# Kernel optimization log

Hardware: AMD Instinct MI355X
Metric: run time of the kernel (lower is better)

The kernel has to match this reference:

```python
import jax, jax.numpy as jnp
import numpy as np


def feature_map(x):
    # phi(x) = elu(x) + 1 (ensures positivity)
    return jax.nn.elu(x) + 1.0


def setup_inputs() -> dict:
    key = jax.random.key(0)
    k0, k1, k2, k3 = jax.random.split(key, 4)
    B, T, d_model, D = 4, 4096, 1024, 128
    x = jax.random.normal(k0, (B, T, d_model), dtype=jnp.float32)
    s = 1.0 / np.sqrt(d_model)
    Wq = jax.random.normal(k1, (d_model, D), dtype=jnp.float32) * s
    Wk = jax.random.normal(k2, (d_model, D), dtype=jnp.float32) * s
    Wv = jax.random.normal(k3, (d_model, D), dtype=jnp.float32) * s
    return {"x": x, "Wq": Wq, "Wk": Wk, "Wv": Wv}


def _causal_linear_attention(phi_q, phi_k, v):
    # phi_q, phi_k: [B,T,D]; v: [B,T,Dv]
    B, T, D = phi_q.shape
    Dv = v.shape[-1]
    # time-major for scan: [T,B,D]
    qT = jnp.swapaxes(phi_q, 0, 1)
    kT = jnp.swapaxes(phi_k, 0, 1)
    vT = jnp.swapaxes(v, 0, 1)

    def step(carry, inp):
        kv, ks = carry                       # kv: [B,D,Dv], ks: [B,D]
        qt, kt, vt = inp                     # each [B,D] / [B,Dv]
        kv = kv + kt[:, :, None] * vt[:, None, :]   # k_t^T v_t outer product
        ks = ks + kt
        num = jnp.einsum('bd,bdv->bv', qt, kv)      # [B,Dv]
        den = jnp.einsum('bd,bd->b', qt, ks)[:, None]
        return (kv, ks), num / den

    init = (jnp.zeros((B, D, Dv), phi_q.dtype), jnp.zeros((B, D), phi_q.dtype))
    _, outT = jax.lax.scan(step, init, (qT, kT, vT))  # outT: [T,B,Dv]
    return jnp.swapaxes(outT, 0, 1)


def reference(x, Wq, Wk, Wv):
    q = x @ Wq
    k = x @ Wk
    v = x @ Wv
    phi_q = feature_map(q)
    phi_k = feature_map(k)
    # dropout is identity in eval mode
    return _causal_linear_attention(phi_q, phi_k, v)
```

## Files before the change

### kernel.cpp

```cpp
#include <hip/hip_runtime.h>

#define DMODEL 1024
#define DHEAD 128
#define CHUNK 128
#define NCHUNK 32

typedef __attribute__((ext_vector_type(4))) float f32x4;
typedef __attribute__((ext_vector_type(8))) short bf16x8;

__device__ __forceinline__ unsigned short f2bf(float f) {
  union { float f; unsigned u; } v; v.f = f;
  unsigned r = v.u + 0x7FFF + ((v.u >> 16) & 1);
  return (unsigned short)(r >> 16);
}
__device__ __forceinline__ float bf2f(unsigned short h) {
  union { unsigned u; float f; } v; v.u = ((unsigned)h) << 16;
  return v.f;
}
__device__ __forceinline__ unsigned cvtpk(float lo, float hi) {
  unsigned r;
  asm("v_cvt_pk_bf16_f32 %0, %1, %2" : "=v"(r) : "v"(lo), "v"(hi));
  return r;
}
__device__ __forceinline__ void gload16(const void* g, void* l) {
  __builtin_amdgcn_global_load_lds(
      (const __attribute__((address_space(1))) unsigned int*)g,
      (__attribute__((address_space(3))) unsigned int*)l, 16, 0, 0);
}

__global__ __launch_bounds__(256) void transpose_w_kernel(
    const float* __restrict__ Wq, const float* __restrict__ Wk,
    const float* __restrict__ Wv, unsigned short* __restrict__ WT) {
  int id = blockIdx.x * 256 + threadIdx.x;
  int w = id >> 17;
  int rem = id & 131071;
  int n = rem >> 10;
  int k = rem & 1023;
  const float* W = (w == 0) ? Wq : (w == 1) ? Wk : Wv;
  WT[id] = f2bf(W[(size_t)k * DHEAD + n]);
}

__global__ __launch_bounds__(256) void proj_kernel(
    const float* __restrict__ x, const unsigned short* __restrict__ WT,
    unsigned short* __restrict__ phiQ, unsigned short* __restrict__ phiK,
    unsigned short* __restrict__ Vb) {
  const int which = blockIdx.y;
  const unsigned short* Wt = WT + (size_t)which * (DHEAD * DMODEL);
  unsigned short* outp = (which == 0) ? phiQ : (which == 1) ? phiK : Vb;
  const int m0 = blockIdx.x * 128;

  __shared__ float xs[128][32];
  __shared__ unsigned short ws[128][32];

  const int tid = threadIdx.x;
  const int wave = tid >> 6;
  const int lane = tid & 63;
  const int lrow = lane & 15, kgrp = lane >> 4;
  const int wr = wave >> 1, wc = wave & 1;

  f32x4 acc[4][4];
#pragma unroll
  for (int i = 0; i < 4; ++i)
#pragma unroll
    for (int j = 0; j < 4; ++j) acc[i][j] = (f32x4)0.0f;

  for (int kk = 0; kk < DMODEL; kk += 32) {
    if (kk) __syncthreads();
#pragma unroll
    for (int i = 0; i < 4; ++i) {
      int instr = i * 4 + wave;
      int row = instr * 8 + (lane >> 3);
      int slot = lane & 7;
      int gcol = (slot ^ (row & 7)) << 2;
      gload16(&x[(size_t)(m0 + row) * DMODEL + kk + gcol],
              (char*)xs + instr * 1024);
    }
#pragma unroll
    for (int i = 0; i < 2; ++i) {
      int instr = i * 4 + wave;
      int row = instr * 16 + (lane >> 2);
      int slot = lane & 3;
      int gcol = (slot ^ (row & 3)) << 3;
      gload16(&Wt[(size_t)row * DMODEL + kk + gcol],
              (char*)ws + instr * 1024);
    }
    __syncthreads();

    bf16x8 af[4];
#pragma unroll
    for (int mi = 0; mi < 4; ++mi) {
      int arow = wr * 64 + mi * 16 + lrow;
      int s0 = kgrp * 2;
      const float4 f0 = *reinterpret_cast<const float4*>(
          &xs[arow][(s0 ^ (arow & 7)) << 2]);
      const float4 f1 = *reinterpret_cast<const float4*>(
          &xs[arow][((s0 + 1) ^ (arow & 7)) << 2]);
      union { unsigned u[4]; bf16x8 v; } p;
      p.u[0] = cvtpk(f0.x, f0.y);
      p.u[1] = cvtpk(f0.z, f0.w);
      p.u[2] = cvtpk(f1.x, f1.y);
      p.u[3] = cvtpk(f1.z, f1.w);
      af[mi] = p.v;
    }
#pragma unroll
    for (int ni = 0; ni < 4; ++ni) {
      int brow = wc * 64 + ni * 16 + lrow;
      bf16x8 bf = *reinterpret_cast<const bf16x8*>(
          &ws[brow][(kgrp ^ (brow & 3)) << 3]);
#pragma unroll
      for (int mi = 0; mi < 4; ++mi)
        acc[mi][ni] = __builtin_amdgcn_mfma_f32_16x16x32_bf16(af[mi], bf, acc[mi][ni], 0, 0, 0);
    }
  }
#pragma unroll
  for (int mi = 0; mi < 4; ++mi)
#pragma unroll
    for (int ni = 0; ni < 4; ++ni)
#pragma unroll
      for (int r = 0; r < 4; ++r) {
        int row = m0 + wr * 64 + mi * 16 + kgrp * 4 + r;
        int col = wc * 64 + ni * 16 + lrow;
        float v = acc[mi][ni][r];
        if (which < 2) v = (v > 0.0f) ? (v + 1.0f) : __expf(v);
        outp[(size_t)row * DHEAD + col] = f2bf(v);
      }
}

__global__ __launch_bounds__(256) void chunkkv_kernel(
    const unsigned short* __restrict__ phiK, const unsigned short* __restrict__ Vb,
    float* __restrict__ KVc, float* __restrict__ ksc) {
  const size_t base = (size_t)blockIdx.x * CHUNK * DHEAD;
  __shared__ unsigned short kt[128][136];
  __shared__ unsigned short vt[128][136];
  __shared__ float csum[2][128];
  const int tid = threadIdx.x;
  const int wave = tid >> 6, lane = tid & 63;
  const int lrow = lane & 15, kgrp = lane >> 4;

  {
    int t = tid & 127, dp = tid >> 7;
#pragma unroll
    for (int i = 0; i < 8; ++i) {
      int d0 = (dp + 2 * i) * 8;
      uint4 k4 = *reinterpret_cast<const uint4*>(&phiK[base + (size_t)t * DHEAD + d0]);
      uint4 v4 = *reinterpret_cast<const uint4*>(&Vb[base + (size_t)t * DHEAD + d0]);
      const unsigned short* kp = reinterpret_cast<const unsigned short*>(&k4);
      const unsigned short* vp = reinterpret_cast<const unsigned short*>(&v4);
#pragma unroll
      for (int j = 0; j < 8; ++j) { kt[d0 + j][t] = kp[j]; vt[d0 + j][t] = vp[j]; }
    }
  }
  __syncthreads();

  f32x4 acc[2][8];
#pragma unroll
  for (int i = 0; i < 2; ++i)
#pragma unroll
    for (int j = 0; j < 8; ++j) acc[i][j] = (f32x4)0.0f;
#pragma unroll
  for (int ks = 0; ks < 4; ++ks) {
    int t0 = ks * 32 + kgrp * 8;
    bf16x8 afrag[2];
#pragma unroll
    for (int tr = 0; tr < 2; ++tr)
      afrag[tr] = *reinterpret_cast<const bf16x8*>(&vt[wave * 32 + tr * 16 + lrow][t0]);
#pragma unroll
    for (int tc = 0; tc < 8; ++tc) {
      bf16x8 bfrag = *reinterpret_cast<const bf16x8*>(&kt[tc * 16 + lrow][t0]);
      acc[0][tc] = __builtin_amdgcn_mfma_f32_16x16x32_bf16(afrag[0], bfrag, acc[0][tc], 0, 0, 0);
      acc[1][tc] = __builtin_amdgcn_mfma_f32_16x16x32_bf16(afrag[1], bfrag, acc[1][tc], 0, 0, 0);
    }
  }
  float* KVout = KVc + (size_t)blockIdx.x * (DHEAD * DHEAD);
#pragma unroll
  for (int tr = 0; tr < 2; ++tr)
#pragma unroll
    for (int tc = 0; tc < 8; ++tc)
#pragma unroll
      for (int r = 0; r < 4; ++r) {
        int dv = wave * 32 + tr * 16 + kgrp * 4 + r;
        int d = tc * 16 + lrow;
        KVout[dv * DHEAD + d] = acc[tr][tc][r];
      }
  {
    int d = tid & 127, hh = tid >> 7;
    float s = 0.0f;
    for (int t = hh * 64; t < hh * 64 + 64; ++t) s += bf2f(kt[d][t]);
    csum[hh][d] = s;
  }
  __syncthreads();
  if (tid < 128) ksc[(size_t)blockIdx.x * DHEAD + tid] = csum[0][tid] + csum[1][tid];
}

__global__ __launch_bounds__(256) void prefix_kernel(
    const float* __restrict__ KVc, const float* __restrict__ ksc,
    unsigned short* __restrict__ KVp, float* __restrict__ ksp) {
  if (blockIdx.x < 256) {
    int id = blockIdx.x * 256 + threadIdx.x;
    int b = id >> 14;
    int e = id & 16383;
    size_t base = (size_t)b * NCHUNK * 16384 + e;
    float acc = 0.0f;
    for (int c = 0; c < NCHUNK; ++c) {
      KVp[base + (size_t)c * 16384] = f2bf(acc);
      acc += KVc[base + (size_t)c * 16384];
    }
  } else {
    for (int i = threadIdx.x; i < 512; i += 256) {
      int b = i >> 7, d = i & 127;
      size_t base = (size_t)b * NCHUNK * DHEAD + d;
      float acc = 0.0f;
      for (int c = 0; c < NCHUNK; ++c) {
        ksp[base + (size_t)c * DHEAD] = acc;
        acc += ksc[base + (size_t)c * DHEAD];
      }
    }
  }
}

__global__ __launch_bounds__(256) void out_kernel(
    const unsigned short* __restrict__ phiQ, const unsigned short* __restrict__ phiK,
    const unsigned short* __restrict__ Vb, const unsigned short* __restrict__ KVp,
    const float* __restrict__ ksp, float* __restrict__ outp) {
  const int c = blockIdx.x;
  const int h = blockIdx.y;
  const size_t kvbase = (size_t)c * CHUNK * DHEAD;
  const size_t qbase = kvbase + (size_t)h * 64 * DHEAD;
  __shared__ unsigned short qb[64][136];
  __shared__ unsigned short kb[128][136];
  __shared__ unsigned short vt[128][136];
  __shared__ float dsum[4][64];
  __shared__ float ks_l[128];
  const int tid = threadIdx.x;
  const int wave = tid >> 6, lane = tid & 63;
  const int lrow = lane & 15, kgrp = lane >> 4;

#pragma unroll
  for (int it = 0; it < 4; ++it) {
    int idx = it * 256 + tid;
    int t = idx >> 4;
    int d0 = (idx & 15) << 3;
    *reinterpret_cast<uint4*>(&qb[t][d0]) =
        *reinterpret_cast<const uint4*>(&phiQ[qbase + (size_t)t * DHEAD + d0]);
  }
  if (tid < 128) ks_l[tid] = ksp[(size_t)c * DHEAD + tid];
  if (h == 0) {
#pragma unroll
    for (int it = 0; it < 4; ++it) {
      int idx = it * 256 + tid;
      int t = idx >> 4;
      int d0 = (idx & 15) << 3;
      *reinterpret_cast<uint4*>(&kb[t][d0]) =
          *reinterpret_cast<const uint4*>(&phiK[kvbase + (size_t)t * DHEAD + d0]);
    }
    int t = tid & 63, dp = tid >> 6;
#pragma unroll
    for (int i = 0; i < 4; ++i) {
      int d0 = (dp + 4 * i) * 8;
      uint4 v4 = *reinterpret_cast<const uint4*>(&Vb[kvbase + (size_t)t * DHEAD + d0]);
      const unsigned short* vp = reinterpret_cast<const unsigned short*>(&v4);
#pragma unroll
      for (int j = 0; j < 8; ++j) vt[d0 + j][t] = vp[j];
    }
  } else {
#pragma unroll
    for (int it = 0; it < 8; ++it) {
      int idx = it * 256 + tid;
      int t = idx >> 4;
      int d0 = (idx & 15) << 3;
      *reinterpret_cast<uint4*>(&kb[t][d0]) =
          *reinterpret_cast<const uint4*>(&phiK[kvbase + (size_t)t * DHEAD + d0]);
    }
    int t = tid & 127, dp = tid >> 7;
#pragma unroll
    for (int i = 0; i < 8; ++i) {
      int d0 = (dp + 2 * i) * 8;
      uint4 v4 = *reinterpret_cast<const uint4*>(&Vb[kvbase + (size_t)t * DHEAD + d0]);
      const unsigned short* vp = reinterpret_cast<const unsigned short*>(&v4);
#pragma unroll
      for (int j = 0; j < 8; ++j) vt[d0 + j][t] = vp[j];
    }
  }
  __syncthreads();

  if (h == 0) {
    f32x4 sa[4];
#pragma unroll
    for (int i = 0; i < 4; ++i) sa[i] = (f32x4)0.0f;
#pragma unroll
    for (int ks = 0; ks < 4; ++ks) {
      int d0 = ks * 32 + kgrp * 8;
      bf16x8 af = *reinterpret_cast<const bf16x8*>(&qb[wave * 16 + lrow][d0]);
#pragma unroll
      for (int tc = 0; tc < 4; ++tc) {
        bf16x8 bf = *reinterpret_cast<const bf16x8*>(&kb[tc * 16 + lrow][d0]);
        sa[tc] = __builtin_amdgcn_mfma_f32_16x16x32_bf16(af, bf, sa[tc], 0, 0, 0);
      }
    }
    __syncthreads();
#pragma unroll
    for (int tc = 0; tc < 4; ++tc)
#pragma unroll
      for (int r = 0; r < 4; ++r) {
        int trow = wave * 16 + kgrp * 4 + r;
        int s = tc * 16 + lrow;
        kb[trow][s] = f2bf((s <= trow) ? sa[tc][r] : 0.0f);
      }
  } else {
    f32x4 sa[8];
#pragma unroll
    for (int i = 0; i < 8; ++i) sa[i] = (f32x4)0.0f;
#pragma unroll
    for (int ks = 0; ks < 4; ++ks) {
      int d0 = ks * 32 + kgrp * 8;
      bf16x8 af = *reinterpret_cast<const bf16x8*>(&qb[wave * 16 + lrow][d0]);
#pragma unroll
      for (int tc = 0; tc < 8; ++tc) {
        bf16x8 bf = *reinterpret_cast<const bf16x8*>(&kb[tc * 16 + lrow][d0]);
        sa[tc] = __builtin_amdgcn_mfma_f32_16x16x32_bf16(af, bf, sa[tc], 0, 0, 0);
      }
    }
    __syncthreads();
#pragma unroll
    for (int tc = 0; tc < 8; ++tc)
#pragma unroll
      for (int r = 0; r < 4; ++r) {
        int trow = wave * 16 + kgrp * 4 + r;
        int s = tc * 16 + lrow;
        kb[trow][s] = f2bf((s <= 64 + trow) ? sa[tc][r] : 0.0f);
      }
  }
  __syncthreads();

  {
    int t = tid & 63, h4 = tid >> 6;
    float s = 0.0f;
    if (h4 < 2) {
      if (h4 == 0 || h == 1) {
        for (int j = h4 * 64; j < h4 * 64 + 64; ++j) s += bf2f(kb[t][j]);
      }
    } else {
      for (int j = (h4 - 2) * 64; j < (h4 - 2) * 64 + 64; ++j)
        s += bf2f(qb[t][j]) * ks_l[j];
    }
    dsum[h4][t] = s;
  }

  f32x4 acc[8];
#pragma unroll
  for (int i = 0; i < 8; ++i) acc[i] = (f32x4)0.0f;
  {
    const int nks = (h == 0) ? 2 : 4;
    for (int ks = 0; ks < nks; ++ks) {
      int t0 = ks * 32 + kgrp * 8;
      bf16x8 af = *reinterpret_cast<const bf16x8*>(&kb[wave * 16 + lrow][t0]);
#pragma unroll
      for (int tc = 0; tc < 8; ++tc) {
        bf16x8 bf = *reinterpret_cast<const bf16x8*>(&vt[tc * 16 + lrow][t0]);
        acc[tc] = __builtin_amdgcn_mfma_f32_16x16x32_bf16(af, bf, acc[tc], 0, 0, 0);
      }
    }
  }
  __syncthreads();

#pragma unroll
  for (int it = 0; it < 8; ++it) {
    int idx = it * 256 + tid;
    int dv = idx >> 4;
    int d0 = (idx & 15) << 3;
    *reinterpret_cast<uint4*>(&vt[dv][d0]) =
        *reinterpret_cast<const uint4*>(&KVp[(size_t)c * 16384 + (size_t)dv * DHEAD + d0]);
  }
  __syncthreads();

#pragma unroll
  for (int ks = 0; ks < 4; ++ks) {
    int d0 = ks * 32 + kgrp * 8;
    bf16x8 af = *reinterpret_cast<const bf16x8*>(&qb[wave * 16 + lrow][d0]);
#pragma unroll
    for (int tc = 0; tc < 8; ++tc) {
      bf16x8 bf = *reinterpret_cast<const bf16x8*>(&vt[tc * 16 + lrow][d0]);
      acc[tc] = __builtin_amdgcn_mfma_f32_16x16x32_bf16(af, bf, acc[tc], 0, 0, 0);
    }
  }

#pragma unroll
  for (int tc = 0; tc < 8; ++tc)
#pragma unroll
    for (int r = 0; r < 4; ++r) {
      int trow = wave * 16 + kgrp * 4 + r;
      int dv = tc * 16 + lrow;
      float den = dsum[0][trow] + dsum[1][trow] + dsum[2][trow] + dsum[3][trow];
      outp[qbase + (size_t)trow * DHEAD + dv] = acc[tc][r] / den;
    }
}

extern "C" void kernel_launch(void* const* d_in, const int* in_sizes, int n_in,
                              void* d_out, int out_size, void* d_ws, size_t ws_size,
                              hipStream_t stream) {
  const float* x  = (const float*)d_in[0];
  const float* Wq = (const float*)d_in[1];
  const float* Wk = (const float*)d_in[2];
  const float* Wv = (const float*)d_in[3];
  float* out = (float*)d_out;
  char* ws = (char*)d_ws;
  unsigned short* phiQ = (unsigned short*)(ws + 0);
  unsigned short* phiK = (unsigned short*)(ws + 4194304);
  unsigned short* Vb   = (unsigned short*)(ws + 8388608);
  unsigned short* WT   = (unsigned short*)(ws + 12582912);
  float*          KVc  = (float*)(ws + 13369344);
  unsigned short* KVp  = (unsigned short*)(ws + 21757952);
  float*          ksc  = (float*)(ws + 25952256);
  float*          ksp  = (float*)(ws + 26017792);

  transpose_w_kernel<<<1536, 256, 0, stream>>>(Wq, Wk, Wv, WT);
  proj_kernel<<<dim3(128, 3), 256, 0, stream>>>(x, WT, phiQ, phiK, Vb);
  chunkkv_kernel<<<128, 256, 0, stream>>>(phiK, Vb, KVc, ksc);
  prefix_kernel<<<257, 256, 0, stream>>>(KVc, ksc, KVp, ksp);
  out_kernel<<<dim3(128, 2), 256, 0, stream>>>(phiQ, phiK, Vb, KVp, ksp, out);
}
```

Baseline: 61.62 us.

## Fuse Q/K/V projections into one block sharing x tile across weights

The projection kernel now computes all three weight projections in each block. It uses a 64x64 output tile per weight and a K step of 64, so each x tile loaded from global memory feeds Q, K and V. Previously x was read three times, once per weight. The grid grows from 384 to 512 blocks with less per-wave M reuse, and each block now keeps 12 accumulators per wave plus larger shared-memory tiles.

After: 57.65 us. -6.4%, faster.

```diff
diff --git a/kernel.cpp b/kernel.cpp
--- a/kernel.cpp
+++ b/kernel.cpp
@@ -44,53 +44,51 @@
     const float* __restrict__ x, const unsigned short* __restrict__ WT,
     unsigned short* __restrict__ phiQ, unsigned short* __restrict__ phiK,
     unsigned short* __restrict__ Vb) {
-  const int which = blockIdx.y;
-  const unsigned short* Wt = WT + (size_t)which * (DHEAD * DMODEL);
-  unsigned short* outp = (which == 0) ? phiQ : (which == 1) ? phiK : Vb;
-  const int m0 = blockIdx.x * 128;
-
-  __shared__ float xs[128][32];
-  __shared__ unsigned short ws[128][32];
+  const int m0 = blockIdx.x * 64;
+  const int n0 = blockIdx.y * 64;
+
+  __shared__ float xs[64][64];
+  __shared__ unsigned short wl[3][64][64];
 
   const int tid = threadIdx.x;
   const int wave = tid >> 6;
   const int lane = tid & 63;
   const int lrow = lane & 15, kgrp = lane >> 4;
-  const int wr = wave >> 1, wc = wave & 1;
-
-  f32x4 acc[4][4];
-#pragma unroll
-  for (int i = 0; i < 4; ++i)
-#pragma unroll
-    for (int j = 0; j < 4; ++j) acc[i][j] = (f32x4)0.0f;
-
-  for (int kk = 0; kk < DMODEL; kk += 32) {
+
+  f32x4 acc[3][4];
+#pragma unroll
+  for (int w3 = 0; w3 < 3; ++w3)
+#pragma unroll
+    for (int j = 0; j < 4; ++j) acc[w3][j] = (f32x4)0.0f;
+
+  for (int kk = 0; kk < DMODEL; kk += 64) {
     if (kk) __syncthreads();
 #pragma unroll
     for (int i = 0; i < 4; ++i) {
       int instr = i * 4 + wave;
-      int row = instr * 8 + (lane >> 3);
-      int slot = lane & 7;
+      int row = instr * 4 + (lane >> 4);
+      int slot = lane & 15;
       int gcol = (slot ^ (row & 7)) << 2;
       gload16(&x[(size_t)(m0 + row) * DMODEL + kk + gcol],
               (char*)xs + instr * 1024);
     }
 #pragma unroll
-    for (int i = 0; i < 2; ++i) {
-      int instr = i * 4 + wave;
-      int row = instr * 16 + (lane >> 2);
-      int slot = lane & 3;
-      int gcol = (slot ^ (row & 3)) << 3;
-      gload16(&Wt[(size_t)row * DMODEL + kk + gcol],
-              (char*)ws + instr * 1024);
+    for (int i = 0; i < 6; ++i) {
+      int j = i * 4 + wave;
+      int w3 = j >> 3;
+      int jj = j & 7;
+      int row = jj * 8 + (lane >> 3);
+      int slot = lane & 7;
+      int gcol = (slot ^ (row & 7)) << 3;
+      gload16(&WT[(size_t)w3 * (DHEAD * DMODEL) + (size_t)(n0 + row) * DMODEL + kk + gcol],
+              (char*)wl + w3 * 8192 + jj * 1024);
     }
     __syncthreads();
 
-    bf16x8 af[4];
-#pragma unroll
-    for (int mi = 0; mi < 4; ++mi) {
-      int arow = wr * 64 + mi * 16 + lrow;
-      int s0 = kgrp * 2;
+#pragma unroll
+    for (int ks2 = 0; ks2 < 2; ++ks2) {
+      int arow = wave * 16 + lrow;
+      int s0 = ks2 * 8 + kgrp * 2;
       const float4 f0 = *reinterpret_cast<const float4*>(
           &xs[arow][(s0 ^ (arow & 7)) << 2]);
       const float4 f1 = *reinterpret_cast<const float4*>(
@@ -100,30 +98,33 @@
       p.u[1] = cvtpk(f0.z, f0.w);
       p.u[2] = cvtpk(f1.x, f1.y);
       p.u[3] = cvtpk(f1.z, f1.w);
-      af[mi] = p.v;
-    }
-#pragma unroll
-    for (int ni = 0; ni < 4; ++ni) {
-      int brow = wc * 64 + ni * 16 + lrow;
-      bf16x8 bf = *reinterpret_cast<const bf16x8*>(
-          &ws[brow][(kgrp ^ (brow & 3)) << 3]);
-#pragma unroll
-      for (int mi = 0; mi < 4; ++mi)
-        acc[mi][ni] = __builtin_amdgcn_mfma_f32_16x16x32_bf16(af[mi], bf, acc[mi][ni], 0, 0, 0);
-    }
-  }
-#pragma unroll
-  for (int mi = 0; mi < 4; ++mi)
-#pragma unroll
-    for (int ni = 0; ni < 4; ++ni)
+      bf16x8 af = p.v;
+#pragma unroll
+      for (int w3 = 0; w3 < 3; ++w3)
+#pragma unroll
+        for (int nt = 0; nt < 4; ++nt) {
+          int brow = nt * 16 + lrow;
+          int bs = ks2 * 4 + kgrp;
+          bf16x8 bf = *reinterpret_cast<const bf16x8*>(
+              &wl[w3][brow][(bs ^ (brow & 7)) << 3]);
+          acc[w3][nt] = __builtin_amdgcn_mfma_f32_16x16x32_bf16(af, bf, acc[w3][nt], 0, 0, 0);
+        }
+    }
+  }
+#pragma unroll
+  for (int w3 = 0; w3 < 3; ++w3) {
+    unsigned short* outp = (w3 == 0) ? phiQ : (w3 == 1) ? phiK : Vb;
+#pragma unroll
+    for (int nt = 0; nt < 4; ++nt)
 #pragma unroll
       for (int r = 0; r < 4; ++r) {
-        int row = m0 + wr * 64 + mi * 16 + kgrp * 4 + r;
-        int col = wc * 64 + ni * 16 + lrow;
-        float v = acc[mi][ni][r];
-        if (which < 2) v = (v > 0.0f) ? (v + 1.0f) : __expf(v);
+        int row = m0 + wave * 16 + kgrp * 4 + r;
+        int col = n0 + nt * 16 + lrow;
+        float v = acc[w3][nt][r];
+        if (w3 < 2) v = (v > 0.0f) ? (v + 1.0f) : __expf(v);
         outp[(size_t)row * DHEAD + col] = f2bf(v);
       }
+  }
 }
 
 __global__ __launch_bounds__(256) void chunkkv_kernel(
@@ -414,7 +415,7 @@
   float*          ksp  = (float*)(ws + 26017792);
 
   transpose_w_kernel<<<1536, 256, 0, stream>>>(Wq, Wk, Wv, WT);
-  proj_kernel<<<dim3(128, 3), 256, 0, stream>>>(x, WT, phiQ, phiK, Vb);
+  proj_kernel<<<dim3(256, 2), 256, 0, stream>>>(x, WT, phiQ, phiK, Vb);
   chunkkv_kernel<<<128, 256, 0, stream>>>(phiK, Vb, KVc, ksc);
   prefix_kernel<<<257, 256, 0, stream>>>(KVc, ksc, KVp, ksp);
   out_kernel<<<dim3(128, 2), 256, 0, stream>>>(phiQ, phiK, Vb, KVp, ksp, out);
```
